# Kernel optimization log

Measured on AMD Instinct MI355X. Metric: run time of the kernel, lower is better.

Reference implementation:

```python
import jax, jax.numpy as jnp
import numpy as np

N, E, G = 51200, 819200, 256            # nodes, directed edges, graphs
N2, A, E2 = 102400, 204800, 409600      # 2-sets, assignments, 2-set edges
D, L, NI2, NAF = 64, 5, 36, 40          # emb_dim, num_layer, num_i_2, num_atom_features
EPS = 1e-5


def _seg_sum(v, seg, n):
    return jax.ops.segment_sum(v, seg, num_segments=n)


def _seg_mean(v, seg, n):
    s = jax.ops.segment_sum(v, seg, num_segments=n)
    c = jax.ops.segment_sum(jnp.ones((v.shape[0],), v.dtype), seg, num_segments=n)
    return s / jnp.maximum(c, 1.0)[:, None]


def setup_inputs() -> dict:
    key = jax.random.key(0)
    ks = iter(jax.random.split(key, 64))
    nrm = lambda shape: jax.random.normal(next(ks), shape, jnp.float32) * 0.1
    x = jax.random.normal(next(ks), (N, NAF), jnp.float32)
    edge_index = jax.random.randint(next(ks), (2, E), 0, N, dtype=jnp.int32)
    edge_attr = jnp.stack([jax.random.randint(next(ks), (E,), 0, 4, dtype=jnp.int32),
                           jax.random.randint(next(ks), (E,), 0, 3, dtype=jnp.int32)], axis=1)
    batch = jnp.repeat(jnp.arange(G, dtype=jnp.int32), N // G)
    iso_type_2 = jax.nn.one_hot(jax.random.randint(next(ks), (N2,), 0, NI2), NI2, dtype=jnp.float32)
    edge_index_2 = jax.random.randint(next(ks), (2, E2), 0, N2, dtype=jnp.int32)
    assignment_index_2 = jnp.stack([jax.random.randint(next(ks), (A,), 0, N, dtype=jnp.int32),
                                    jnp.repeat(jnp.arange(N2, dtype=jnp.int32), 2)], axis=0)
    batch_2 = jnp.repeat(jnp.arange(G, dtype=jnp.int32), N2 // G)
    params = dict(
        emb_W=nrm((NAF, D)), emb_b=jnp.zeros((D,), jnp.float32),
        gin_W1=nrm((L, D, 2 * D)), gin_b1=jnp.zeros((L, 2 * D), jnp.float32),
        gin_W2=nrm((L, 2 * D, D)), gin_b2=jnp.zeros((L, D), jnp.float32),
        eemb1=nrm((L, 6, D)), eemb2=nrm((L, 3, D)),
        bn_gamma=jnp.ones((L, D), jnp.float32), bn_beta=jnp.zeros((L, D), jnp.float32),
        iso1_rel_W=nrm((D + NI2, D)), iso1_rel_b=jnp.zeros((D,), jnp.float32),
        iso1_root_W=nrm((D + NI2, D)),
        iso2_rel_W=nrm((D, D)), iso2_rel_b=jnp.zeros((D,), jnp.float32),
        iso2_root_W=nrm((D, D)),
        ro_W0=nrm((2 * D, D)), ro_b0=jnp.zeros((D,), jnp.float32),
        ro_W1=nrm((D, D // 2)), ro_b1=jnp.zeros((D // 2,), jnp.float32),
        ro_W2=nrm((D // 2, D // 4)), ro_b2=jnp.zeros((D // 4,), jnp.float32),
        last_W=nrm((D // 4, 1)), last_b=jnp.zeros((1,), jnp.float32),
    )
    return dict(x=x, edge_index=edge_index, edge_attr=edge_attr, batch=batch,
                iso_type_2=iso_type_2, edge_index_2=edge_index_2,
                assignment_index_2=assignment_index_2, batch_2=batch_2, **params)


def _forward(x, iso_type_2, emb_W, emb_b, gin_W1, gin_b1, gin_W2, gin_b2,
             eemb1, eemb2, bn_gamma, bn_beta,
             iso1_rel_W, iso1_rel_b, iso1_root_W, iso2_rel_W, iso2_rel_b, iso2_root_W,
             ro_W0, ro_b0, ro_W1, ro_b1, ro_W2, ro_b2, last_W, last_b,
             edge_index, edge_attr, batch, edge_index_2, assignment_index_2, batch_2):
    # --- GIN stack with edge-feature embeddings and self loops ---
    loop = jnp.arange(N, dtype=edge_index.dtype)
    src = jnp.concatenate([edge_index[0], loop])
    dst = jnp.concatenate([edge_index[1], loop])
    sl_attr = jnp.tile(jnp.array([[4, 0]], dtype=edge_attr.dtype), (N, 1))
    ea = jnp.concatenate([edge_attr, sl_attr], axis=0)  # [E+N, 2]

    h = jax.nn.relu(x @ emb_W + emb_b)  # x_embedding1
    for l in range(L):
        e = eemb1[l][ea[:, 0]] + eemb2[l][ea[:, 1]]      # [E+N, D]
        agg = _seg_sum(h[src] + e, dst, N)               # gather + scatter-add
        h2 = jax.nn.relu(agg @ gin_W1[l] + gin_b1[l]) @ gin_W2[l] + gin_b2[l]
        mu = jnp.mean(h2, axis=0)
        var = jnp.var(h2, axis=0)                        # biased, torch BN training mode
        h2 = (h2 - mu) / jnp.sqrt(var + EPS) * bn_gamma[l] + bn_beta[l]
        h = h2 if l == L - 1 else jax.nn.relu(h2)        # last layer: no ReLU (JK='last')
    node_rep = h

    # --- graph mean pool of node representation ---
    x1 = _seg_mean(node_rep, batch, G)                   # [G, D]

    # --- 2-set branch: avg_pool onto 2-sets, concat iso type, two GraphConvs ---
    xp = _seg_mean(node_rep[assignment_index_2[0]], assignment_index_2[1], N2)
    xp = jnp.concatenate([xp, iso_type_2], axis=1)       # [N2, D+NI2]

    def graph_conv(z, Wrel, brel, Wroot):
        agg = _seg_sum(z[edge_index_2[0]], edge_index_2[1], N2)
        return agg @ Wrel + brel + z @ Wroot

    xp = jax.nn.relu(graph_conv(xp, iso1_rel_W, iso1_rel_b, iso1_root_W))
    xp = jax.nn.relu(graph_conv(xp, iso2_rel_W, iso2_rel_b, iso2_root_W))
    x2 = _seg_mean(xp, batch_2, G)                       # [G, D]

    # --- readout MLP ---
    m = jnp.concatenate([x1, x2], axis=1)                # [G, 2D]
    m = jax.nn.relu(m @ ro_W0 + ro_b0)
    m = jax.nn.relu(m @ ro_W1 + ro_b1)
    m = jax.nn.relu(m @ ro_W2 + ro_b2)
    m = m @ last_W + last_b
    return m.reshape(-1)                                 # num_tasks == 1 -> flat [G]


def reference(x, edge_index, edge_attr, batch, iso_type_2, edge_index_2,
              assignment_index_2, batch_2, emb_W, emb_b, gin_W1, gin_b1, gin_W2,
              gin_b2, eemb1, eemb2, bn_gamma, bn_beta, iso1_rel_W, iso1_rel_b,
              iso1_root_W, iso2_rel_W, iso2_rel_b, iso2_root_W, ro_W0, ro_b0,
              ro_W1, ro_b1, ro_W2, ro_b2, last_W, last_b):
    return _forward(x, iso_type_2, emb_W, emb_b, gin_W1, gin_b1, gin_W2, gin_b2,
                    eemb1, eemb2, bn_gamma, bn_beta,
                    iso1_rel_W, iso1_rel_b, iso1_root_W, iso2_rel_W, iso2_rel_b,
                    iso2_root_W, ro_W0, ro_b0, ro_W1, ro_b1, ro_W2, ro_b2,
                    last_W, last_b, edge_index, edge_attr, batch, edge_index_2,
                    assignment_index_2, batch_2)
```

## Files before the change

kernel.cpp:

```cpp
#include <hip/hip_runtime.h>

#define NN   51200
#define EE   819200
#define GG   256
#define NN2  102400
#define AA   204800
#define EE2  409600
#define DD   64
#define LL   5

#define NB1  100
#define NB2  200
#define CAP1 10240
#define CAP2 3072

typedef __attribute__((ext_vector_type(8))) short bf16x8;
typedef __attribute__((ext_vector_type(4))) float f32x4;
typedef unsigned short ushort_t;

#define OFF_H      ((size_t)0)
#define OFF_AGG    ((size_t)13107200)
#define OFF_H2     ((size_t)26214400)
#define OFF_XP     ((size_t)39321600)
#define OFF_REC1   OFF_XP
#define OFF_REC2   ((size_t)47513600)
#define OFF_PERM   ((size_t)60293120)
#define OFF_YROOT  ((size_t)65536000)
#define OFF_OFFS1  ((size_t)91750400)
#define OFF_COL1   ((size_t)91955216)
#define OFF_OFFS2  ((size_t)95232016)
#define OFF_COL2   ((size_t)95641632)
#define OFF_CNT1   ((size_t)97280032)
#define OFF_BBASE  ((size_t)97282080)
#define OFF_CUR1   ((size_t)97484832)
#define OFF_STATS  ((size_t)98508832)
#define ZERO_BYTES ((size_t)1231360)
#define OFF_ISO    ((size_t)98511392)
#define OFF_M      ((size_t)98920992)
#define WS_NEEDED  ((size_t)99052064)

__device__ __forceinline__ int waveInclScan(int v, int lane) {
#pragma unroll
    for (int off = 1; off < 64; off <<= 1) {
        int t = __shfl_up(v, off, 64);
        if (lane >= off) v += t;
    }
    return v;
}

__device__ __forceinline__ void bsplit(float x, ushort_t& hi, ushort_t& lo) {
    union { float f; unsigned u; } a; a.f = x;
    unsigned hb = (a.u + 0x7FFFu + ((a.u >> 16) & 1u)) >> 16;
    union { unsigned u; float f; } h; h.u = hb << 16;
    float r = x - h.f;
    union { float f; unsigned u; } b; b.f = r;
    unsigned lb = (b.u + 0x7FFFu + ((b.u >> 16) & 1u)) >> 16;
    hi = (ushort_t)hb; lo = (ushort_t)lb;
}

__global__ __launch_bounds__(256) void kbA(const int* __restrict__ src1, const int* __restrict__ dst1,
                                           const int* __restrict__ ea,
                                           const int* __restrict__ src2, const int* __restrict__ dst2,
                                           int* __restrict__ bucketCnt,
                                           int2* __restrict__ rec1, int2* __restrict__ rec2) {
    __shared__ int lhist[256];
    __shared__ int lbase[256];
    int tid = threadIdx.x, b = blockIdx.x;
    lhist[tid] = 0;
    __syncthreads();
    if (b < 400) {
        int i = (b * 256 + tid) * 8;
        int4 d0 = *(const int4*)(dst1 + i);
        int4 d1 = *(const int4*)(dst1 + i + 4);
        int dst[8] = {d0.x, d0.y, d0.z, d0.w, d1.x, d1.y, d1.z, d1.w};
        int bin[8], lr[8];
#pragma unroll
        for (int j = 0; j < 8; ++j) {
            bin[j] = dst[j] >> 9;
            lr[j] = atomicAdd(&lhist[bin[j]], 1);
        }
        __syncthreads();
        if (tid < NB1) {
            int c = lhist[tid];
            lbase[tid] = c ? atomicAdd(&bucketCnt[tid], c) : 0;
        }
        __syncthreads();
        int4 s0 = *(const int4*)(src1 + i);
        int4 s1 = *(const int4*)(src1 + i + 4);
        int src[8] = {s0.x, s0.y, s0.z, s0.w, s1.x, s1.y, s1.z, s1.w};
        int4 e0 = *(const int4*)(ea + 2 * i);
        int4 e1 = *(const int4*)(ea + 2 * i + 4);
        int4 e2 = *(const int4*)(ea + 2 * i + 8);
        int4 e3 = *(const int4*)(ea + 2 * i + 12);
        int code[8] = {e0.x * 3 + e0.y, e0.z * 3 + e0.w, e1.x * 3 + e1.y, e1.z * 3 + e1.w,
                       e2.x * 3 + e2.y, e2.z * 3 + e2.w, e3.x * 3 + e3.y, e3.z * 3 + e3.w};
#pragma unroll
        for (int j = 0; j < 8; ++j) {
            int pos = bin[j] * CAP1 + lbase[bin[j]] + lr[j];
            rec1[pos] = make_int2(src[j] | (code[j] << 16), dst[j]);
        }
    } else {
        int i = ((b - 400) * 256 + tid) * 8;
        int4 d0 = *(const int4*)(dst2 + i);
        int4 d1 = *(const int4*)(dst2 + i + 4);
        int dst[8] = {d0.x, d0.y, d0.z, d0.w, d1.x, d1.y, d1.z, d1.w};
        int bin[8], lr[8];
#pragma unroll
        for (int j = 0; j < 8; ++j) {
            bin[j] = dst[j] >> 9;
            lr[j] = atomicAdd(&lhist[bin[j]], 1);
        }
        __syncthreads();
        if (tid < NB2) {
            int c = lhist[tid];
            lbase[tid] = c ? atomicAdd(&bucketCnt[NB1 + tid], c) : 0;
        }
        __syncthreads();
        int4 s0 = *(const int4*)(src2 + i);
        int4 s1 = *(const int4*)(src2 + i + 4);
        int src[8] = {s0.x, s0.y, s0.z, s0.w, s1.x, s1.y, s1.z, s1.w};
#pragma unroll
        for (int j = 0; j < 8; ++j) {
            int pos = bin[j] * CAP2 + lbase[bin[j]] + lr[j];
            rec2[pos] = make_int2(src[j], dst[j]);
        }
    }
}

__global__ void kbscan(const int* __restrict__ bucketCnt, int* __restrict__ bucketBase) {
    __shared__ int wsum[4];
    int tid = threadIdx.x, lane = tid & 63, wid = tid >> 6;
    int nb = blockIdx.x ? NB2 : NB1;
    const int* cnt = bucketCnt + (blockIdx.x ? NB1 : 0);
    int* base = bucketBase + (blockIdx.x ? NB1 : 0);
    int v = (tid < nb) ? cnt[tid] : 0;
    int incl = waveInclScan(v, lane);
    if (lane == 63) wsum[wid] = incl;
    __syncthreads();
    int woff = 0;
#pragma unroll
    for (int w = 0; w < 3; ++w) woff += (w < wid) ? wsum[w] : 0;
    if (tid < nb) base[tid] = woff + incl - v;
}

__global__ __launch_bounds__(256) void kbB(const int* __restrict__ bucketCnt,
                                           const int* __restrict__ bucketBase,
                                           const int2* __restrict__ rec1, const int2* __restrict__ rec2,
                                           int* __restrict__ offs1, int* __restrict__ col1,
                                           int* __restrict__ offs2, int* __restrict__ col2,
                                           int* __restrict__ dbin) {
    __shared__ int nh[512];
    __shared__ int ncur[512];
    __shared__ int wsum[4];
    __shared__ int dhist[64];
    int tid = threadIdx.x, b = blockIdx.x;
    bool g1 = b < NB1;
    const int2* rec = g1 ? (rec1 + (size_t)b * CAP1) : (rec2 + (size_t)(b - NB1) * CAP2);
    int cnt = bucketCnt[b];
    int base = bucketBase[b];
    int* offs = g1 ? offs1 : offs2;
    int* col = g1 ? col1 : col2;
    int nodeBase = g1 ? b * 512 : (b - NB1) * 512;
    nh[tid] = 0; nh[tid + 256] = 0;
    if (tid < 64) dhist[tid] = 0;
    __syncthreads();
    for (int e = tid; e < cnt; e += 256) {
        int2 r = rec[e];
        atomicAdd(&nh[r.y & 511], 1);
    }
    __syncthreads();
    int v0 = nh[2 * tid], v1 = nh[2 * tid + 1];
    int s = v0 + v1;
    int lane = tid & 63, wid = tid >> 6;
    int incl = waveInclScan(s, lane);
    if (lane == 63) wsum[wid] = incl;
    __syncthreads();
    int woff = 0;
#pragma unroll
    for (int w = 0; w < 3; ++w) woff += (w < wid) ? wsum[w] : 0;
    int excl = woff + incl - s;
    ncur[2 * tid] = excl;
    ncur[2 * tid + 1] = excl + v0;
    offs[nodeBase + 2 * tid] = base + excl;
    offs[nodeBase + 2 * tid + 1] = base + excl + v0;
    if (g1) {
        atomicAdd(&dhist[v0 < 63 ? v0 : 63], 1);
        atomicAdd(&dhist[v1 < 63 ? v1 : 63], 1);
    }
    __syncthreads();
    for (int e = tid; e < cnt; e += 256) {
        int2 r = rec[e];
        int node = r.y & 511;
        int slot = base + atomicAdd(&ncur[node], 1);
        col[slot] = r.x;
    }
    if (g1 && tid < 64 && dhist[tid]) atomicAdd(&dbin[tid], dhist[tid]);
    if (tid == 0) {
        if (b == NB1 - 1) offs1[NN] = EE;
        if (b == NB1 + NB2 - 1) offs2[NN2] = EE2;
    }
}

__global__ __launch_bounds__(256) void kiso(const float* __restrict__ iso, int* __restrict__ isoIdx) {
    __shared__ float srow[256 * 36];
    int tid = threadIdx.x;
    int base = blockIdx.x * 256;
    const float4* g4p = (const float4*)(iso + (size_t)base * 36);
#pragma unroll
    for (int i = tid; i < 2304; i += 256) ((float4*)srow)[i] = g4p[i];
    __syncthreads();
    const float* r = srow + tid * 36;
    int best = 0;
#pragma unroll
    for (int k = 0; k < 36; ++k)
        if (r[k] > 0.5f) best = k;
    isoIdx[base + tid] = best;
}

__global__ void kprepx(const float* __restrict__ x, const float* __restrict__ embW,
                       const float* __restrict__ embB, float* __restrict__ h,
                       const float* __restrict__ gW1, const float* __restrict__ gW2,
                       ushort_t* __restrict__ w1h, ushort_t* __restrict__ w1l,
                       ushort_t* __restrict__ w2h, ushort_t* __restrict__ w2l,
                       const float* __restrict__ i1rW, const float* __restrict__ i1tW,
                       const float* __restrict__ i2rW, const float* __restrict__ i2tW,
                       ushort_t* __restrict__ gcwh, ushort_t* __restrict__ gcwl) {
    int b = blockIdx.x;
    if (b < 12800) {
        int t = b * 256 + threadIdx.x;
        int n = t >> 6, d = t & 63;
        float acc = embB[d];
        const float4* xr4 = (const float4*)(x + (size_t)n * 40);
#pragma unroll
        for (int k4 = 0; k4 < 10; ++k4) {
            float4 xv = xr4[k4];
            acc = fmaf(xv.x, embW[(4 * k4 + 0) * 64 + d], acc);
            acc = fmaf(xv.y, embW[(4 * k4 + 1) * 64 + d], acc);
            acc = fmaf(xv.z, embW[(4 * k4 + 2) * 64 + d], acc);
            acc = fmaf(xv.w, embW[(4 * k4 + 3) * 64 + d], acc);
        }
        h[(size_t)n * 64 + d] = fmaxf(acc, 0.f);
    } else if (b < 12840) {
        int t = (b - 12800) * 256 + threadIdx.x;
        int lane = t & 63, frag = t >> 6;
        int c15 = lane & 15, q = lane >> 4;
        if (frag < 80) {
            int kt = frag & 1, nt = (frag >> 1) & 7, l = frag >> 4;
            const float* W = gW1 + l * 8192;
            ushort_t* oh = w1h + ((size_t)frag * 64 + lane) * 8;
            ushort_t* ol = w1l + ((size_t)frag * 64 + lane) * 8;
            int kb = kt * 32 + q * 8, colw = nt * 16 + c15;
#pragma unroll
            for (int j = 0; j < 8; ++j) {
                ushort_t hi, lo; bsplit(W[(kb + j) * 128 + colw], hi, lo);
                oh[j] = hi; ol[j] = lo;
            }
        } else if (frag < 160) {
            int f = frag - 80;
            int kt = f & 3, nt = (f >> 2) & 3, l = f >> 4;
            const float* W = gW2 + l * 8192;
            ushort_t* oh = w2h + ((size_t)f * 64 + lane) * 8;
            ushort_t* ol = w2l + ((size_t)f * 64 + lane) * 8;
            int kb = kt * 32 + q * 8, colw = nt * 16 + c15;
#pragma unroll
            for (int j = 0; j < 8; ++j) {
                ushort_t hi, lo; bsplit(W[(kb + j) * 64 + colw], hi, lo);
                oh[j] = hi; ol[j] = lo;
            }
        }
    } else {
        int t = (b - 12840) * 256 + threadIdx.x;
        int lane = t & 63, frag = t >> 6;
        int c15 = lane & 15, q = lane >> 4;
        int m = frag >> 3, f = frag & 7;
        int kt = f & 1, nt = f >> 1;
        const float* W = (m == 0) ? i1rW : (m == 1) ? i1tW : (m == 2) ? i2rW : i2tW;
        ushort_t* oh = gcwh + (size_t)m * 4096 + ((size_t)f * 64 + lane) * 8;
        ushort_t* ol = gcwl + (size_t)m * 4096 + ((size_t)f * 64 + lane) * 8;
        int kb = kt * 32 + q * 8, colw = nt * 16 + c15;
#pragma unroll
        for (int j = 0; j < 8; ++j) {
            ushort_t hi, lo; bsplit(W[(kb + j) * 64 + colw], hi, lo);
            oh[j] = hi; ol[j] = lo;
        }
    }
}

__global__ __launch_bounds__(256) void kdegplace(const int* __restrict__ offs,
                                                 const int* __restrict__ dbin,
                                                 int* __restrict__ dcur,
                                                 int* __restrict__ perm) {
    __shared__ int lhist[64];
    __shared__ int lbase[64];
    __shared__ int sdstart[64];
    int tid = threadIdx.x;
    if (tid < 64) {
        lhist[tid] = 0;
        int v = dbin[tid];
        int incl = waveInclScan(v, tid);
        sdstart[tid] = incl - v;
    }
    __syncthreads();
    int n = blockIdx.x * 256 + tid;
    int d = offs[n + 1] - offs[n]; d = d < 63 ? d : 63;
    int lr = atomicAdd(&lhist[d], 1);
    __syncthreads();
    if (tid < 64) {
        int c = lhist[tid];
        lbase[tid] = c ? atomicAdd(&dcur[tid], c) : 0;
    }
    __syncthreads();
    perm[sdstart[d] + lbase[d] + lr] = n;
}

__global__ __launch_bounds__(256) void ktrans(float* __restrict__ h,
                                              const float* __restrict__ pst,
                                              const float* __restrict__ gamma,
                                              const float* __restrict__ beta) {
    __shared__ float sstat[128];
    __shared__ float sSC[64], sSH[64];
    int tid = threadIdx.x;
    if (tid < 128) {
        float s = 0.f;
        const float* p = pst + tid;
#pragma unroll
        for (int i = 0; i < 32; ++i) s += p[i * 128];
        sstat[tid] = s;
    }
    __syncthreads();
    if (tid < 64) {
        float mu = sstat[tid] * (1.f / NN);
        float var = sstat[64 + tid] * (1.f / NN) - mu * mu;
        float sc = gamma[tid] * rsqrtf(var + 1e-5f);
        sSC[tid] = sc; sSH[tid] = beta[tid] - mu * sc;
    }
    __syncthreads();
    int c = (tid & 15) * 4;
    float4 sc4 = *(const float4*)(sSC + c);
    float4 sh4 = *(const float4*)(sSH + c);
    float4* hp = (float4*)h;
    size_t base = (size_t)blockIdx.x * 1024 + tid;
#pragma unroll
    for (int r = 0; r < 4; ++r) {
        float4 v = hp[base + r * 256];
        v.x = fmaxf(fmaf(v.x, sc4.x, sh4.x), 0.f);
        v.y = fmaxf(fmaf(v.y, sc4.y, sh4.y), 0.f);
        v.z = fmaxf(fmaf(v.z, sc4.z, sh4.z), 0.f);
        v.w = fmaxf(fmaf(v.w, sc4.w, sh4.w), 0.f);
        hp[base + r * 256] = v;
    }
}

__global__ __launch_bounds__(256) void kglayer(
    const float* __restrict__ hin, float* __restrict__ hout,
    const int* __restrict__ perm,
    const int* __restrict__ offs, const int* __restrict__ col,
    const float* __restrict__ e1, const float* __restrict__ e2,
    const ushort_t* __restrict__ w1h, const ushort_t* __restrict__ w1l,
    const ushort_t* __restrict__ w2h, const ushort_t* __restrict__ w2l,
    const float* __restrict__ b1, const float* __restrict__ b2,
    float* __restrict__ pstout) {
    __shared__ float etab[13 * 64];
    __shared__ int sPerm[16];
    __shared__ float sMLP[16 * 132];
    float* sA = sMLP;
    float* sH = sMLP;
    int tid = threadIdx.x;
    if (tid < 16) sPerm[tid] = perm[blockIdx.x * 16 + tid];
    for (int idx = tid; idx < 13 * 64; idx += 256) {
        int ci = idx >> 6, dd = idx & 63;
        etab[idx] = e1[(ci / 3) * 64 + dd] + e2[(ci % 3) * 64 + dd];
    }
    __syncthreads();
    int lane = tid & 63, wv = tid >> 6;
    int c15 = lane & 15, q = lane >> 4;

    {
        int n = sPerm[wv * 4 + q];
        int s0 = offs[n], s1 = offs[n + 1];
        float4 sx = *(const float4*)(hin + (size_t)n * 64 + 4 * c15);
        float4 et = *(const float4*)(etab + 12 * 64 + 4 * c15);
        float a0 = sx.x + et.x, a1 = sx.y + et.y, a2 = sx.z + et.z, a3 = sx.w + et.w;
        int deg = s1 - s0;
        if (deg > 0) {
            const int* cp = col + s0;
            int nfull = deg >> 3, rem = deg & 7;
            int vv[8];
#pragma unroll
            for (int j = 0; j < 8; ++j) {
                int idx = j < deg ? j : deg - 1;
                vv[j] = cp[idx];
            }
            for (int it = 0; it < nfull; ++it) {
                float4 xv[8], tv[8];
#pragma unroll
                for (int j = 0; j < 8; ++j) {
                    xv[j] = *(const float4*)(hin + (size_t)(vv[j] & 0xFFFF) * 64 + 4 * c15);
                    tv[j] = *(const float4*)(etab + (vv[j] >> 16) * 64 + 4 * c15);
                }
                int e8 = (it + 1) * 8;
                bool more = e8 < deg;
                int nx[8];
                if (more) {
#pragma unroll
                    for (int j = 0; j < 8; ++j) {
                        int idx = e8 + j; idx = idx < deg ? idx : deg - 1;
                        nx[j] = cp[idx];
                    }
                }
#pragma unroll
                for (int j = 0; j < 8; ++j) {
                    a0 += xv[j].x + tv[j].x;
                    a1 += xv[j].y + tv[j].y;
                    a2 += xv[j].z + tv[j].z;
                    a3 += xv[j].w + tv[j].w;
                }
                if (more) {
#pragma unroll
                    for (int j = 0; j < 8; ++j) vv[j] = nx[j];
                }
            }
            if (rem) {
                float4 xv[8], tv[8];
#pragma unroll
                for (int j = 0; j < 8; ++j) {
                    xv[j] = *(const float4*)(hin + (size_t)(vv[j] & 0xFFFF) * 64 + 4 * c15);
                    tv[j] = *(const float4*)(etab + (vv[j] >> 16) * 64 + 4 * c15);
                }
#pragma unroll
                for (int j = 0; j < 8; ++j) {
                    float mm = (j < rem) ? 1.f : 0.f;
                    a0 = fmaf(xv[j].x + tv[j].x, mm, a0);
                    a1 = fmaf(xv[j].y + tv[j].y, mm, a1);
                    a2 = fmaf(xv[j].z + tv[j].z, mm, a2);
                    a3 = fmaf(xv[j].w + tv[j].w, mm, a3);
                }
            }
        }
        *(float4*)(sA + (wv * 4 + q) * 68 + 4 * c15) = make_float4(a0, a1, a2, a3);
    }
    __syncthreads();

    bf16x8 ah[2], al[2];
#pragma unroll
    for (int kt = 0; kt < 2; ++kt) {
        const float* p = sA + c15 * 68 + kt * 32 + q * 8;
        float4 x0 = *(const float4*)p;
        float4 x1 = *(const float4*)(p + 4);
        float xs[8] = {x0.x, x0.y, x0.z, x0.w, x1.x, x1.y, x1.z, x1.w};
#pragma unroll
        for (int j = 0; j < 8; ++j) {
            ushort_t hi, lo; bsplit(xs[j], hi, lo);
            ah[kt][j] = (short)hi; al[kt][j] = (short)lo;
        }
    }
    __syncthreads();

    f32x4 acc1[2];
#pragma unroll
    for (int j = 0; j < 2; ++j) { f32x4 z = {0.f, 0.f, 0.f, 0.f}; acc1[j] = z; }
#pragma unroll
    for (int kt = 0; kt < 2; ++kt) {
#pragma unroll
        for (int j = 0; j < 2; ++j) {
            int nt = 2 * wv + j;
            size_t fo = ((size_t)((nt * 2 + kt) * 64 + lane)) * 8;
            bf16x8 bh = *(const bf16x8*)(w1h + fo);
            bf16x8 bl = *(const bf16x8*)(w1l + fo);
            acc1[j] = __builtin_amdgcn_mfma_f32_16x16x32_bf16(ah[kt], bh, acc1[j], 0, 0, 0);
            acc1[j] = __builtin_amdgcn_mfma_f32_16x16x32_bf16(al[kt], bh, acc1[j], 0, 0, 0);
            acc1[j] = __builtin_amdgcn_mfma_f32_16x16x32_bf16(ah[kt], bl, acc1[j], 0, 0, 0);
        }
    }
#pragma unroll
    for (int j = 0; j < 2; ++j) {
        int nt = 2 * wv + j;
        float bias = b1[nt * 16 + c15];
#pragma unroll
        for (int rg = 0; rg < 4; ++rg)
            sH[(4 * q + rg) * 132 + nt * 16 + c15] = fmaxf(acc1[j][rg] + bias, 0.f);
    }
    __syncthreads();

    f32x4 acc2 = {0.f, 0.f, 0.f, 0.f};
#pragma unroll
    for (int kt = 0; kt < 4; ++kt) {
        const float* p = sH + c15 * 132 + kt * 32 + q * 8;
        float4 x0 = *(const float4*)p;
        float4 x1 = *(const float4*)(p + 4);
        float xs[8] = {x0.x, x0.y, x0.z, x0.w, x1.x, x1.y, x1.z, x1.w};
        bf16x8 a2h, a2l;
#pragma unroll
        for (int j = 0; j < 8; ++j) {
            ushort_t hi, lo; bsplit(xs[j], hi, lo);
            a2h[j] = (short)hi; a2l[j] = (short)lo;
        }
        size_t fo = ((size_t)((wv * 4 + kt) * 64 + lane)) * 8;
        bf16x8 bh = *(const bf16x8*)(w2h + fo);
        bf16x8 bl = *(const bf16x8*)(w2l + fo);
        acc2 = __builtin_amdgcn_mfma_f32_16x16x32_bf16(a2h, bh, acc2, 0, 0, 0);
        acc2 = __builtin_amdgcn_mfma_f32_16x16x32_bf16(a2l, bh, acc2, 0, 0, 0);
        acc2 = __builtin_amdgcn_mfma_f32_16x16x32_bf16(a2h, bl, acc2, 0, 0, 0);
    }
    {
        float bias = b2[wv * 16 + c15];
        float s = 0.f, s2 = 0.f;
#pragma unroll
        for (int rg = 0; rg < 4; ++rg) {
            float v = acc2[rg] + bias;
            hout[(size_t)sPerm[4 * q + rg] * 64 + wv * 16 + c15] = v;
            s += v; s2 += v * v;
        }
        s += __shfl_xor(s, 16, 64);  s += __shfl_xor(s, 32, 64);
        s2 += __shfl_xor(s2, 16, 64); s2 += __shfl_xor(s2, 32, 64);
        if (q == 0) {
            float* ps = pstout + (size_t)(blockIdx.x & 31) * 128;
            atomicAdd(&ps[wv * 16 + c15], s);
            atomicAdd(&ps[64 + wv * 16 + c15], s2);
        }
    }
}

__global__ __launch_bounds__(256) void kgcmm1(const ushort_t* __restrict__ grh,
                                              const ushort_t* __restrict__ grl,
                                              const ushort_t* __restrict__ gth,
                                              const ushort_t* __restrict__ gtl,
                                              const float* __restrict__ WrelIso,
                                              const float* __restrict__ WrootIso,
                                              const int* __restrict__ isoIdx,
                                              float* __restrict__ Yrel,
                                              float* __restrict__ Yroot,
                                              const float* __restrict__ pst,
                                              const float* __restrict__ g4,
                                              const float* __restrict__ b4,
                                              const int* __restrict__ a0g,
                                              const float* __restrict__ h2src) {
    __shared__ float sX[64 * 68];
    __shared__ float sstat[128];
    __shared__ float sSC[64], sSH[64];
    int tid = threadIdx.x, blk = blockIdx.x;
    if (tid < 128) {
        float s = 0.f;
        const float* p = pst + tid;
#pragma unroll
        for (int i = 0; i < 32; ++i) s += p[i * 128];
        sstat[tid] = s;
    }
    __syncthreads();
    if (tid < 64) {
        float mu = sstat[tid] * (1.f / NN);
        float var = sstat[64 + tid] * (1.f / NN) - mu * mu;
        float sc = g4[tid] * rsqrtf(var + 1e-5f);
        sSC[tid] = sc;
        sSH[tid] = b4[tid] - mu * sc;
    }
    __syncthreads();
#pragma unroll
    for (int i = tid; i < 1024; i += 256) {
        int row = i >> 4, c = (i & 15) << 2;
        int grow = blk * 64 + row;
        int na = a0g[2 * grow], nb = a0g[2 * grow + 1];
        float4 va = *(const float4*)(h2src + (size_t)na * 64 + c);
        float4 vb = *(const float4*)(h2src + (size_t)nb * 64 + c);
        float4 v;
        v.x = 0.5f * (va.x + vb.x); v.y = 0.5f * (va.y + vb.y);
        v.z = 0.5f * (va.z + vb.z); v.w = 0.5f * (va.w + vb.w);
        v.x = fmaf(v.x, sSC[c], sSH[c]);
        v.y = fmaf(v.y, sSC[c + 1], sSH[c + 1]);
        v.z = fmaf(v.z, sSC[c + 2], sSH[c + 2]);
        v.w = fmaf(v.w, sSC[c + 3], sSH[c + 3]);
        float* p = sX + row * 68 + c;
        p[0] = v.x; p[1] = v.y; p[2] = v.z; p[3] = v.w;
    }
    __syncthreads();
    int lane = tid & 63, wv = tid >> 6;
    int c15 = lane & 15, q = lane >> 4;

    bf16x8 ah[2], al[2];
#pragma unroll
    for (int kt = 0; kt < 2; ++kt) {
        const float* p = sX + (16 * wv + c15) * 68 + kt * 32 + q * 8;
        float4 x0 = *(const float4*)p;
        float4 x1 = *(const float4*)(p + 4);
        float xs[8] = {x0.x, x0.y, x0.z, x0.w, x1.x, x1.y, x1.z, x1.w};
#pragma unroll
        for (int j = 0; j < 8; ++j) {
            ushort_t hi, lo; bsplit(xs[j], hi, lo);
            ah[kt][j] = (short)hi; al[kt][j] = (short)lo;
        }
    }

    f32x4 accR[4], accT[4];
#pragma unroll
    for (int nt = 0; nt < 4; ++nt) {
        f32x4 z = {0.f, 0.f, 0.f, 0.f};
        accR[nt] = z; accT[nt] = z;
    }
#pragma unroll
    for (int nt = 0; nt < 4; ++nt) {
#pragma unroll
        for (int kt = 0; kt < 2; ++kt) {
            size_t fo = ((size_t)((nt * 2 + kt) * 64 + lane)) * 8;
            bf16x8 bh = *(const bf16x8*)(grh + fo);
            bf16x8 bl = *(const bf16x8*)(grl + fo);
            accR[nt] = __builtin_amdgcn_mfma_f32_16x16x32_bf16(ah[kt], bh, accR[nt], 0, 0, 0);
            accR[nt] = __builtin_amdgcn_mfma_f32_16x16x32_bf16(al[kt], bh, accR[nt], 0, 0, 0);
            accR[nt] = __builtin_amdgcn_mfma_f32_16x16x32_bf16(ah[kt], bl, accR[nt], 0, 0, 0);
            bf16x8 ch = *(const bf16x8*)(gth + fo);
            bf16x8 cl = *(const bf16x8*)(gtl + fo);
            accT[nt] = __builtin_amdgcn_mfma_f32_16x16x32_bf16(ah[kt], ch, accT[nt], 0, 0, 0);
            accT[nt] = __builtin_amdgcn_mfma_f32_16x16x32_bf16(al[kt], ch, accT[nt], 0, 0, 0);
            accT[nt] = __builtin_amdgcn_mfma_f32_16x16x32_bf16(ah[kt], cl, accT[nt], 0, 0, 0);
        }
    }

    int rbase = blk * 64 + 16 * wv + 4 * q;
#pragma unroll
    for (int rg = 0; rg < 4; ++rg) {
        int row = rbase + rg;
        int ii = isoIdx[row];
        float* yr = Yrel + (size_t)row * 64;
        float* yt = Yroot + (size_t)row * 64;
        const float* er = WrelIso + (size_t)ii * 64;
        const float* et = WrootIso + (size_t)ii * 64;
#pragma unroll
        for (int nt = 0; nt < 4; ++nt) {
            int cc = nt * 16 + c15;
            yr[cc] = accR[nt][rg] + er[cc];
            yt[cc] = accT[nt][rg] + et[cc];
        }
    }
}

__global__ __launch_bounds__(256) void kgcmm2(const float* __restrict__ AGG,
                                              const float* __restrict__ XP,
                                              const ushort_t* __restrict__ grh,
                                              const ushort_t* __restrict__ grl,
                                              const ushort_t* __restrict__ gth,
                                              const ushort_t* __restrict__ gtl,
                                              const float* __restrict__ brel,
                                              float* __restrict__ OUT) {
    __shared__ float sA[64 * 68];
    __shared__ float sB[64 * 68];
    int tid = threadIdx.x, blk = blockIdx.x;
#pragma unroll
    for (int i = tid; i < 1024; i += 256) {
        int row = i >> 4, c = (i & 15) << 2;
        float4 va = ((const float4*)(AGG + (size_t)blk * 4096))[i];
        float4 vb = ((const float4*)(XP + (size_t)blk * 4096))[i];
        float* pa = sA + row * 68 + c;
        float* pb = sB + row * 68 + c;
        pa[0] = va.x; pa[1] = va.y; pa[2] = va.z; pa[3] = va.w;
        pb[0] = vb.x; pb[1] = vb.y; pb[2] = vb.z; pb[3] = vb.w;
    }
    __syncthreads();
    int lane = tid & 63, wv = tid >> 6;
    int c15 = lane & 15, q = lane >> 4;

    bf16x8 aAh[2], aAl[2], aBh[2], aBl[2];
#pragma unroll
    for (int kt = 0; kt < 2; ++kt) {
        const float* pa = sA + (16 * wv + c15) * 68 + kt * 32 + q * 8;
        const float* pb = sB + (16 * wv + c15) * 68 + kt * 32 + q * 8;
        float4 a0 = *(const float4*)pa;
        float4 a1 = *(const float4*)(pa + 4);
        float4 b0 = *(const float4*)pb;
        float4 b1 = *(const float4*)(pb + 4);
        float as[8] = {a0.x, a0.y, a0.z, a0.w, a1.x, a1.y, a1.z, a1.w};
        float bs[8] = {b0.x, b0.y, b0.z, b0.w, b1.x, b1.y, b1.z, b1.w};
#pragma unroll
        for (int j = 0; j < 8; ++j) {
            ushort_t hi, lo;
            bsplit(as[j], hi, lo); aAh[kt][j] = (short)hi; aAl[kt][j] = (short)lo;
            bsplit(bs[j], hi, lo); aBh[kt][j] = (short)hi; aBl[kt][j] = (short)lo;
        }
    }

    f32x4 acc[4];
#pragma unroll
    for (int nt = 0; nt < 4; ++nt) { f32x4 z = {0.f, 0.f, 0.f, 0.f}; acc[nt] = z; }
#pragma unroll
    for (int nt = 0; nt < 4; ++nt) {
#pragma unroll
        for (int kt = 0; kt < 2; ++kt) {
            size_t fo = ((size_t)((nt * 2 + kt) * 64 + lane)) * 8;
            bf16x8 bh = *(const bf16x8*)(grh + fo);
            bf16x8 bl = *(const bf16x8*)(grl + fo);
            acc[nt] = __builtin_amdgcn_mfma_f32_16x16x32_bf16(aAh[kt], bh, acc[nt], 0, 0, 0);
            acc[nt] = __builtin_amdgcn_mfma_f32_16x16x32_bf16(aAl[kt], bh, acc[nt], 0, 0, 0);
            acc[nt] = __builtin_amdgcn_mfma_f32_16x16x32_bf16(aAh[kt], bl, acc[nt], 0, 0, 0);
            bf16x8 ch = *(const bf16x8*)(gth + fo);
            bf16x8 cl = *(const bf16x8*)(gtl + fo);
            acc[nt] = __builtin_amdgcn_mfma_f32_16x16x32_bf16(aBh[kt], ch, acc[nt], 0, 0, 0);
            acc[nt] = __builtin_amdgcn_mfma_f32_16x16x32_bf16(aBl[kt], ch, acc[nt], 0, 0, 0);
            acc[nt] = __builtin_amdgcn_mfma_f32_16x16x32_bf16(aBh[kt], cl, acc[nt], 0, 0, 0);
        }
    }

    int rbase = blk * 64 + 16 * wv + 4 * q;
#pragma unroll
    for (int rg = 0; rg < 4; ++rg) {
        int row = rbase + rg;
        float* yo = OUT + (size_t)row * 64;
#pragma unroll
        for (int nt = 0; nt < 4; ++nt) {
            int cc = nt * 16 + c15;
            yo[cc] = fmaxf(acc[nt][rg] + brel[cc], 0.f);
        }
    }
}

__global__ void kgather2(const float* __restrict__ yrel, const float* __restrict__ yroot,
                         const float* __restrict__ brel, const int* __restrict__ offs,
                         const int* __restrict__ col, float* __restrict__ out) {
    int t = blockIdx.x * 256 + threadIdx.x;
    int j = t >> 4, c = t & 15;
    int s0 = offs[j], s1 = offs[j + 1];
    float4 rt = *(const float4*)(yroot + (size_t)j * 64 + 4 * c);
    float4 bb = *(const float4*)(brel + 4 * c);
    float a0 = rt.x + bb.x, a1 = rt.y + bb.y, a2 = rt.z + bb.z, a3 = rt.w + bb.w;
    if (s0 < s1) {
        int vv[4];
#pragma unroll
        for (int jj = 0; jj < 4; ++jj) {
            int idx = s0 + jj; idx = idx < s1 ? idx : s1 - 1;
            vv[jj] = col[idx];
        }
        int e = s0;
        while (true) {
            int ne = e + 4;
            bool more = ne < s1;
            float4 xs[4];
#pragma unroll
            for (int jj = 0; jj < 4; ++jj)
                xs[jj] = *(const float4*)(yrel + (size_t)vv[jj] * 64 + 4 * c);
            int nx[4];
            if (more) {
#pragma unroll
                for (int jj = 0; jj < 4; ++jj) {
                    int idx = ne + jj; idx = idx < s1 ? idx : s1 - 1;
                    nx[jj] = col[idx];
                }
            }
#pragma unroll
            for (int jj = 0; jj < 4; ++jj) {
                float mm = (e + jj < s1) ? 1.f : 0.f;
                a0 = fmaf(xs[jj].x, mm, a0);
                a1 = fmaf(xs[jj].y, mm, a1);
                a2 = fmaf(xs[jj].z, mm, a2);
                a3 = fmaf(xs[jj].w, mm, a3);
            }
            if (!more) break;
            e = ne;
#pragma unroll
            for (int jj = 0; jj < 4; ++jj) vv[jj] = nx[jj];
        }
    }
    *(float4*)(out + (size_t)j * 64 + 4 * c) =
        make_float4(fmaxf(a0, 0.f), fmaxf(a1, 0.f), fmaxf(a2, 0.f), fmaxf(a3, 0.f));
}

__global__ void kgather2raw(const float* __restrict__ xpsrc, const int* __restrict__ offs,
                            const int* __restrict__ col, float* __restrict__ agg) {
    int t = blockIdx.x * 256 + threadIdx.x;
    int j = t >> 4, c = t & 15;
    int s0 = offs[j], s1 = offs[j + 1];
    float a0 = 0.f, a1 = 0.f, a2 = 0.f, a3 = 0.f;
    if (s0 < s1) {
        int vv[4];
#pragma unroll
        for (int jj = 0; jj < 4; ++jj) {
            int idx = s0 + jj; idx = idx < s1 ? idx : s1 - 1;
            vv[jj] = col[idx];
        }
        int e = s0;
        while (true) {
            int ne = e + 4;
            bool more = ne < s1;
            float4 xs[4];
#pragma unroll
            for (int jj = 0; jj < 4; ++jj)
                xs[jj] = *(const float4*)(xpsrc + (size_t)vv[jj] * 64 + 4 * c);
            int nx[4];
            if (more) {
#pragma unroll
                for (int jj = 0; jj < 4; ++jj) {
                    int idx = ne + jj; idx = idx < s1 ? idx : s1 - 1;
                    nx[jj] = col[idx];
                }
            }
#pragma unroll
            for (int jj = 0; jj < 4; ++jj) {
                float mm = (e + jj < s1) ? 1.f : 0.f;
                a0 = fmaf(xs[jj].x, mm, a0);
                a1 = fmaf(xs[jj].y, mm, a1);
                a2 = fmaf(xs[jj].z, mm, a2);
                a3 = fmaf(xs[jj].w, mm, a3);
            }
            if (!more) break;
            e = ne;
#pragma unroll
            for (int jj = 0; jj < 4; ++jj) vv[jj] = nx[jj];
        }
    }
    *(float4*)(agg + (size_t)j * 64 + 4 * c) = make_float4(a0, a1, a2, a3);
}

__global__ void kpoolg(const float* __restrict__ h2, const float* __restrict__ xp2,
                       const float* __restrict__ pst, const float* __restrict__ g4,
                       const float* __restrict__ b4, float* __restrict__ m) {
    __shared__ float sstat[128];
    __shared__ float red[4][64];
    int g = blockIdx.x, tid = threadIdx.x;
    if (tid < 128) {
        float s = 0.f;
        const float* p = pst + tid;
#pragma unroll
        for (int i = 0; i < 32; ++i) s += p[i * 128];
        sstat[tid] = s;
    }
    int wid = tid >> 6, d = tid & 63;
    float s1 = 0.f;
    for (int i = wid; i < 200; i += 4) s1 += h2[((size_t)g * 200 + i) * 64 + d];
    red[wid][d] = s1;
    __syncthreads();
    if (wid == 0) {
        float mean = (red[0][d] + red[1][d] + red[2][d] + red[3][d]) * (1.f / 200.f);
        float mu = sstat[d] * (1.f / NN);
        float var = sstat[64 + d] * (1.f / NN) - mu * mu;
        float sc = g4[d] * rsqrtf(var + 1e-5f);
        m[g * 128 + d] = fmaf(mean, sc, b4[d] - mu * sc);
    }
    __syncthreads();
    float s2 = 0.f;
    for (int i = wid; i < 400; i += 4) s2 += xp2[((size_t)g * 400 + i) * 64 + d];
    red[wid][d] = s2;
    __syncthreads();
    if (wid == 0) m[g * 128 + 64 + d] = (red[0][d] + red[1][d] + red[2][d] + red[3][d]) * (1.f / 400.f);
}

__global__ void kread(const float* __restrict__ m, const float* __restrict__ W0,
                      const float* __restrict__ b0, const float* __restrict__ W1,
                      const float* __restrict__ b1, const float* __restrict__ W2,
                      const float* __restrict__ b2, const float* __restrict__ lw,
                      const float* __restrict__ lb, float* __restrict__ out) {
    __shared__ float s0[64], s1[32], s2[16];
    int g = blockIdx.x, d = threadIdx.x;
    const float* mr = m + g * 128;
    float t = b0[d];
    for (int k = 0; k < 128; ++k) t = fmaf(mr[k], W0[k * 64 + d], t);
    s0[d] = fmaxf(t, 0.f);
    __syncthreads();
    if (d < 32) {
        float u = b1[d];
        for (int k = 0; k < 64; ++k) u = fmaf(s0[k], W1[k * 32 + d], u);
        s1[d] = fmaxf(u, 0.f);
    }
    __syncthreads();
    if (d < 16) {
        float u = b2[d];
        for (int k = 0; k < 32; ++k) u = fmaf(s1[k], W2[k * 16 + d], u);
        s2[d] = fmaxf(u, 0.f);
    }
    __syncthreads();
    if (d == 0) {
        float u = lb[0];
        for (int k = 0; k < 16; ++k) u = fmaf(s2[k], lw[k], u);
        out[g] = u;
    }
}

extern "C" void kernel_launch(void* const* d_in, const int* in_sizes, int n_in,
                              void* d_out, int out_size, void* d_ws, size_t ws_size,
                              hipStream_t stream) {
    if (ws_size < WS_NEEDED) return;

    const float* x    = (const float*)d_in[0];
    const int*   ei   = (const int*)d_in[1];
    const int*   ea   = (const int*)d_in[2];
    const float* iso  = (const float*)d_in[4];
    const int*   ei2  = (const int*)d_in[5];
    const int*   ai2  = (const int*)d_in[6];
    const float* embW = (const float*)d_in[8];
    const float* embB = (const float*)d_in[9];
    const float* gW1  = (const float*)d_in[10];
    const float* gB1  = (const float*)d_in[11];
    const float* gW2  = (const float*)d_in[12];
    const float* gB2  = (const float*)d_in[13];
    const float* ee1  = (const float*)d_in[14];
    const float* ee2  = (const float*)d_in[15];
    const float* bng  = (const float*)d_in[16];
    const float* bnb  = (const float*)d_in[17];
    const float* i1rW = (const float*)d_in[18];
    const float* i1rB = (const float*)d_in[19];
    const float* i1tW = (const float*)d_in[20];
    const float* i2rW = (const float*)d_in[21];
    const float* i2rB = (const float*)d_in[22];
    const float* i2tW = (const float*)d_in[23];
    const float* roW0 = (const float*)d_in[24];
    const float* roB0 = (const float*)d_in[25];
    const float* roW1 = (const float*)d_in[26];
    const float* roB1 = (const float*)d_in[27];
    const float* roW2 = (const float*)d_in[28];
    const float* roB2 = (const float*)d_in[29];
    const float* lW   = (const float*)d_in[30];
    const float* lB   = (const float*)d_in[31];
    float* out = (float*)d_out;

    char* ws = (char*)d_ws;
    float* h      = (float*)(ws + OFF_H);
    float* hB     = (float*)(ws + OFF_AGG);
    float* hA     = (float*)(ws + OFF_H2);
    float* h2     = hA;
    float* xp     = (float*)(ws + OFF_XP);
    float* yrel   = (float*)(ws + OFF_H);
    float* yroot  = (float*)(ws + OFF_YROOT);
    float* aggb   = (float*)(ws + OFF_H);
    float* xp2    = (float*)(ws + OFF_YROOT);
    int* offs1    = (int*)(ws + OFF_OFFS1);
    int* col1     = (int*)(ws + OFF_COL1);
    int* offs2    = (int*)(ws + OFF_OFFS2);
    int* col2     = (int*)(ws + OFF_COL2);
    int* isoIdx   = (int*)(ws + OFF_ISO);
    float* mbuf   = (float*)(ws + OFF_M);
    ushort_t* w1h = (ushort_t*)(ws + OFF_YROOT);
    ushort_t* w1l = (ushort_t*)(ws + OFF_YROOT + 81920);
    ushort_t* w2h = (ushort_t*)(ws + OFF_YROOT + 163840);
    ushort_t* w2l = (ushort_t*)(ws + OFF_YROOT + 245760);
    ushort_t* gcwh = (ushort_t*)(ws + OFF_M);
    ushort_t* gcwl = (ushort_t*)(ws + OFF_M + 32768);
    float* pstat2 = (float*)(ws + OFF_CUR1);
    int2* rec1    = (int2*)(ws + OFF_REC1);
    int2* rec2    = (int2*)(ws + OFF_REC2);
    int* bucketCnt  = (int*)(ws + OFF_CNT1);
    int* bucketBase = (int*)(ws + OFF_BBASE);
    int* perm     = (int*)(ws + OFF_PERM);
    int* dbin     = (int*)(ws + OFF_STATS);
    int* dcur     = dbin + 64;

    const int* src1 = ei;
    const int* dst1 = ei + EE;
    const int* src2 = ei2;
    const int* dst2 = ei2 + EE2;
    const int* a0   = ai2;

    hipMemsetAsync(ws + OFF_CNT1, 0, ZERO_BYTES, stream);

    kbA<<<600, 256, 0, stream>>>(src1, dst1, ea, src2, dst2, bucketCnt, rec1, rec2);
    kiso<<<NN2 / 256, 256, 0, stream>>>(iso, isoIdx);
    kprepx<<<12848, 256, 0, stream>>>(x, embW, embB, h, gW1, gW2,
                                      w1h, w1l, w2h, w2l,
                                      i1rW, i1tW, i2rW, i2tW, gcwh, gcwl);
    kbscan<<<2, 256, 0, stream>>>(bucketCnt, bucketBase);
    kbB<<<300, 256, 0, stream>>>(bucketCnt, bucketBase, rec1, rec2,
                                 offs1, col1, offs2, col2, dbin);
    kdegplace<<<NN / 256, 256, 0, stream>>>(offs1, dbin, dcur, perm);

    for (int l = 0; l < LL; ++l) {
        const float* hin = (l == 0) ? h : ((l & 1) ? hA : hB);
        float* hout = (l & 1) ? hB : hA;
        kglayer<<<NN / 16, 256, 0, stream>>>(
            hin, hout, perm, offs1, col1, ee1 + l * 384, ee2 + l * 192,
            w1h + (size_t)l * 8192, w1l + (size_t)l * 8192,
            w2h + (size_t)l * 8192, w2l + (size_t)l * 8192,
            gB1 + l * 128, gB2 + l * 64,
            pstat2 + (size_t)l * 4096);
        if (l < LL - 1)
            ktrans<<<800, 256, 0, stream>>>(hout, pstat2 + (size_t)l * 4096,
                                            bng + l * 64, bnb + l * 64);
    }

    kgcmm1<<<NN2 / 64, 256, 0, stream>>>(gcwh, gcwl, gcwh + 4096, gcwl + 4096,
                                         i1rW + 64 * 64, i1tW + 64 * 64, isoIdx,
                                         yrel, yroot,
                                         pstat2 + (size_t)4 * 4096,
                                         bng + 4 * 64, bnb + 4 * 64, a0, h2);
    kgather2<<<NN2 * 16 / 256, 256, 0, stream>>>(yrel, yroot, i1rB, offs2, col2, xp);
    kgather2raw<<<NN2 * 16 / 256, 256, 0, stream>>>(xp, offs2, col2, aggb);
    kgcmm2<<<NN2 / 64, 256, 0, stream>>>(aggb, xp,
                                         gcwh + 8192, gcwl + 8192, gcwh + 12288, gcwl + 12288,
                                         i2rB, xp2);

    kpoolg<<<GG, 256, 0, stream>>>(h2, xp2, pstat2 + (size_t)4 * 4096,
                                   bng + 4 * 64, bnb + 4 * 64, mbuf);
    kread<<<GG, 64, 0, stream>>>(mbuf, roW0, roB0, roW1, roB1, roW2, roB2, lW, lB, out);
}
```

Baseline: 568.3 us.

## Store gathered node features in bf16 to halve gather traffic

Result: faster. 529.3 us (-6.9%).

```diff
diff --git a/kernel.cpp b/kernel.cpp
--- a/kernel.cpp
+++ b/kernel.cpp
@@ -57,6 +57,13 @@
     unsigned lb = (b.u + 0x7FFFu + ((b.u >> 16) & 1u)) >> 16;
     hi = (ushort_t)hb; lo = (ushort_t)lb;
 }
+__device__ __forceinline__ ushort_t f2bf(float x) {
+    union { float f; unsigned u; } a; a.f = x;
+    return (ushort_t)((a.u + 0x7FFFu + ((a.u >> 16) & 1u)) >> 16);
+}
+__device__ __forceinline__ float bf2f(ushort_t v) {
+    union { unsigned u; float f; } t; t.u = (unsigned)v << 16; return t.f;
+}
 
 __global__ __launch_bounds__(256) void kbA(const int* __restrict__ src1, const int* __restrict__ dst1,
                                            const int* __restrict__ ea,
@@ -218,7 +225,7 @@
 }
 
 __global__ void kprepx(const float* __restrict__ x, const float* __restrict__ embW,
-                       const float* __restrict__ embB, float* __restrict__ h,
+                       const float* __restrict__ embB, ushort_t* __restrict__ hbf,
                        const float* __restrict__ gW1, const float* __restrict__ gW2,
                        ushort_t* __restrict__ w1h, ushort_t* __restrict__ w1l,
                        ushort_t* __restrict__ w2h, ushort_t* __restrict__ w2l,
@@ -239,7 +246,7 @@
             acc = fmaf(xv.z, embW[(4 * k4 + 2) * 64 + d], acc);
             acc = fmaf(xv.w, embW[(4 * k4 + 3) * 64 + d], acc);
         }
-        h[(size_t)n * 64 + d] = fmaxf(acc, 0.f);
+        hbf[(size_t)n * 64 + d] = f2bf(fmaxf(acc, 0.f));
     } else if (b < 12840) {
         int t = (b - 12800) * 256 + threadIdx.x;
         int lane = t & 63, frag = t >> 6;
@@ -313,7 +320,8 @@
     perm[sdstart[d] + lbase[d] + lr] = n;
 }
 
-__global__ __launch_bounds__(256) void ktrans(float* __restrict__ h,
+__global__ __launch_bounds__(256) void ktrans(const float* __restrict__ hraw,
+                                              ushort_t* __restrict__ hbf,
                                               const float* __restrict__ pst,
                                               const float* __restrict__ gamma,
                                               const float* __restrict__ beta) {
@@ -338,21 +346,23 @@
     int c = (tid & 15) * 4;
     float4 sc4 = *(const float4*)(sSC + c);
     float4 sh4 = *(const float4*)(sSH + c);
-    float4* hp = (float4*)h;
+    const float4* hp = (const float4*)hraw;
+    ushort4* op = (ushort4*)hbf;
     size_t base = (size_t)blockIdx.x * 1024 + tid;
 #pragma unroll
     for (int r = 0; r < 4; ++r) {
         float4 v = hp[base + r * 256];
-        v.x = fmaxf(fmaf(v.x, sc4.x, sh4.x), 0.f);
-        v.y = fmaxf(fmaf(v.y, sc4.y, sh4.y), 0.f);
-        v.z = fmaxf(fmaf(v.z, sc4.z, sh4.z), 0.f);
-        v.w = fmaxf(fmaf(v.w, sc4.w, sh4.w), 0.f);
-        hp[base + r * 256] = v;
+        ushort4 o;
+        o.x = f2bf(fmaxf(fmaf(v.x, sc4.x, sh4.x), 0.f));
+        o.y = f2bf(fmaxf(fmaf(v.y, sc4.y, sh4.y), 0.f));
+        o.z = f2bf(fmaxf(fmaf(v.z, sc4.z, sh4.z), 0.f));
+        o.w = f2bf(fmaxf(fmaf(v.w, sc4.w, sh4.w), 0.f));
+        op[base + r * 256] = o;
     }
 }
 
 __global__ __launch_bounds__(256) void kglayer(
-    const float* __restrict__ hin, float* __restrict__ hout,
+    const ushort_t* __restrict__ hin, float* __restrict__ hout,
     const int* __restrict__ perm,
     const int* __restrict__ offs, const int* __restrict__ col,
     const float* __restrict__ e1, const float* __restrict__ e2,
@@ -378,9 +388,10 @@
     {
         int n = sPerm[wv * 4 + q];
         int s0 = offs[n], s1 = offs[n + 1];
-        float4 sx = *(const float4*)(hin + (size_t)n * 64 + 4 * c15);
+        ushort4 sx = *(const ushort4*)(hin + (size_t)n * 64 + 4 * c15);
         float4 et = *(const float4*)(etab + 12 * 64 + 4 * c15);
-        float a0 = sx.x + et.x, a1 = sx.y + et.y, a2 = sx.z + et.z, a3 = sx.w + et.w;
+        float a0 = bf2f(sx.x) + et.x, a1 = bf2f(sx.y) + et.y;
+        float a2 = bf2f(sx.z) + et.z, a3 = bf2f(sx.w) + et.w;
         int deg = s1 - s0;
         if (deg > 0) {
             const int* cp = col + s0;
@@ -392,10 +403,11 @@
                 vv[j] = cp[idx];
             }
             for (int it = 0; it < nfull; ++it) {
-                float4 xv[8], tv[8];
+                ushort4 xv[8];
+                float4 tv[8];
 #pragma unroll
                 for (int j = 0; j < 8; ++j) {
-                    xv[j] = *(const float4*)(hin + (size_t)(vv[j] & 0xFFFF) * 64 + 4 * c15);
+                    xv[j] = *(const ushort4*)(hin + (size_t)(vv[j] & 0xFFFF) * 64 + 4 * c15);
                     tv[j] = *(const float4*)(etab + (vv[j] >> 16) * 64 + 4 * c15);
                 }
                 int e8 = (it + 1) * 8;
@@ -410,10 +422,10 @@
                 }
 #pragma unroll
                 for (int j = 0; j < 8; ++j) {
-                    a0 += xv[j].x + tv[j].x;
-                    a1 += xv[j].y + tv[j].y;
-                    a2 += xv[j].z + tv[j].z;
-                    a3 += xv[j].w + tv[j].w;
+                    a0 += bf2f(xv[j].x) + tv[j].x;
+                    a1 += bf2f(xv[j].y) + tv[j].y;
+                    a2 += bf2f(xv[j].z) + tv[j].z;
+                    a3 += bf2f(xv[j].w) + tv[j].w;
                 }
                 if (more) {
 #pragma unroll
@@ -421,19 +433,20 @@
                 }
             }
             if (rem) {
-                float4 xv[8], tv[8];
+                ushort4 xv[8];
+                float4 tv[8];
 #pragma unroll
                 for (int j = 0; j < 8; ++j) {
-                    xv[j] = *(const float4*)(hin + (size_t)(vv[j] & 0xFFFF) * 64 + 4 * c15);
+                    xv[j] = *(const ushort4*)(hin + (size_t)(vv[j] & 0xFFFF) * 64 + 4 * c15);
                     tv[j] = *(const float4*)(etab + (vv[j] >> 16) * 64 + 4 * c15);
                 }
 #pragma unroll
                 for (int j = 0; j < 8; ++j) {
                     float mm = (j < rem) ? 1.f : 0.f;
-                    a0 = fmaf(xv[j].x + tv[j].x, mm, a0);
-                    a1 = fmaf(xv[j].y + tv[j].y, mm, a1);
-                    a2 = fmaf(xv[j].z + tv[j].z, mm, a2);
-                    a3 = fmaf(xv[j].w + tv[j].w, mm, a3);
+                    a0 = fmaf(bf2f(xv[j].x) + tv[j].x, mm, a0);
+                    a1 = fmaf(bf2f(xv[j].y) + tv[j].y, mm, a1);
+                    a2 = fmaf(bf2f(xv[j].z) + tv[j].z, mm, a2);
+                    a3 = fmaf(bf2f(xv[j].w) + tv[j].w, mm, a3);
                 }
             }
         }
@@ -528,7 +541,7 @@
                                               const float* __restrict__ WrelIso,
                                               const float* __restrict__ WrootIso,
                                               const int* __restrict__ isoIdx,
-                                              float* __restrict__ Yrel,
+                                              ushort_t* __restrict__ Yrel,
                                               float* __restrict__ Yroot,
                                               const float* __restrict__ pst,
                                               const float* __restrict__ g4,
@@ -619,21 +632,21 @@
     for (int rg = 0; rg < 4; ++rg) {
         int row = rbase + rg;
         int ii = isoIdx[row];
-        float* yr = Yrel + (size_t)row * 64;
+        ushort_t* yr = Yrel + (size_t)row * 64;
         float* yt = Yroot + (size_t)row * 64;
         const float* er = WrelIso + (size_t)ii * 64;
         const float* et = WrootIso + (size_t)ii * 64;
 #pragma unroll
         for (int nt = 0; nt < 4; ++nt) {
             int cc = nt * 16 + c15;
-            yr[cc] = accR[nt][rg] + er[cc];
+            yr[cc] = f2bf(accR[nt][rg] + er[cc]);
             yt[cc] = accT[nt][rg] + et[cc];
         }
     }
 }
 
 __global__ __launch_bounds__(256) void kgcmm2(const float* __restrict__ AGG,
-                                              const float* __restrict__ XP,
+                                              const ushort_t* __restrict__ XP,
                                               const ushort_t* __restrict__ grh,
                                               const ushort_t* __restrict__ grl,
                                               const ushort_t* __restrict__ gth,
@@ -647,17 +660,17 @@
     for (int i = tid; i < 1024; i += 256) {
         int row = i >> 4, c = (i & 15) << 2;
         float4 va = ((const float4*)(AGG + (size_t)blk * 4096))[i];
-        float4 vb = ((const float4*)(XP + (size_t)blk * 4096))[i];
+        ushort4 vb4 = ((const ushort4*)(XP + (size_t)blk * 4096))[i];
         float* pa = sA + row * 68 + c;
         float* pb = sB + row * 68 + c;
         pa[0] = va.x; pa[1] = va.y; pa[2] = va.z; pa[3] = va.w;
-        pb[0] = vb.x; pb[1] = vb.y; pb[2] = vb.z; pb[3] = vb.w;
+        pb[0] = bf2f(vb4.x); pb[1] = bf2f(vb4.y); pb[2] = bf2f(vb4.z); pb[3] = bf2f(vb4.w);
     }
     __syncthreads();
     int lane = tid & 63, wv = tid >> 6;
     int c15 = lane & 15, q = lane >> 4;
 
-    bf16x8 aAh[2], aAl[2], aBh[2], aBl[2];
+    bf16x8 aAh[2], aAl[2], aBh[2];
 #pragma unroll
     for (int kt = 0; kt < 2; ++kt) {
         const float* pa = sA + (16 * wv + c15) * 68 + kt * 32 + q * 8;
@@ -672,7 +685,7 @@
         for (int j = 0; j < 8; ++j) {
             ushort_t hi, lo;
             bsplit(as[j], hi, lo); aAh[kt][j] = (short)hi; aAl[kt][j] = (short)lo;
-            bsplit(bs[j], hi, lo); aBh[kt][j] = (short)hi; aBl[kt][j] = (short)lo;
+            aBh[kt][j] = (short)f2bf(bs[j]);
         }
     }
 
@@ -692,7 +705,6 @@
             bf16x8 ch = *(const bf16x8*)(gth + fo);
             bf16x8 cl = *(const bf16x8*)(gtl + fo);
             acc[nt] = __builtin_amdgcn_mfma_f32_16x16x32_bf16(aBh[kt], ch, acc[nt], 0, 0, 0);
-            acc[nt] = __builtin_amdgcn_mfma_f32_16x16x32_bf16(aBl[kt], ch, acc[nt], 0, 0, 0);
             acc[nt] = __builtin_amdgcn_mfma_f32_16x16x32_bf16(aBh[kt], cl, acc[nt], 0, 0, 0);
         }
     }
@@ -710,9 +722,9 @@
     }
 }
 
-__global__ void kgather2(const float* __restrict__ yrel, const float* __restrict__ yroot,
+__global__ void kgather2(const ushort_t* __restrict__ yrel, const float* __restrict__ yroot,
                          const float* __restrict__ brel, const int* __restrict__ offs,
-                         const int* __restrict__ col, float* __restrict__ out) {
+                         const int* __restrict__ col, ushort_t* __restrict__ out) {
     int t = blockIdx.x * 256 + threadIdx.x;
     int j = t >> 4, c = t & 15;
     int s0 = offs[j], s1 = offs[j + 1];
@@ -730,10 +742,10 @@
         while (true) {
             int ne = e + 4;
             bool more = ne < s1;
-            float4 xs[4];
+            ushort4 xs[4];
 #pragma unroll
             for (int jj = 0; jj < 4; ++jj)
-                xs[jj] = *(const float4*)(yrel + (size_t)vv[jj] * 64 + 4 * c);
+                xs[jj] = *(const ushort4*)(yrel + (size_t)vv[jj] * 64 + 4 * c);
             int nx[4];
             if (more) {
 #pragma unroll
@@ -745,10 +757,10 @@
 #pragma unroll
             for (int jj = 0; jj < 4; ++jj) {
                 float mm = (e + jj < s1) ? 1.f : 0.f;
-                a0 = fmaf(xs[jj].x, mm, a0);
-                a1 = fmaf(xs[jj].y, mm, a1);
-                a2 = fmaf(xs[jj].z, mm, a2);
-                a3 = fmaf(xs[jj].w, mm, a3);
+                a0 = fmaf(bf2f(xs[jj].x), mm, a0);
+                a1 = fmaf(bf2f(xs[jj].y), mm, a1);
+                a2 = fmaf(bf2f(xs[jj].z), mm, a2);
+                a3 = fmaf(bf2f(xs[jj].w), mm, a3);
             }
             if (!more) break;
             e = ne;
@@ -756,11 +768,15 @@
             for (int jj = 0; jj < 4; ++jj) vv[jj] = nx[jj];
         }
     }
-    *(float4*)(out + (size_t)j * 64 + 4 * c) =
-        make_float4(fmaxf(a0, 0.f), fmaxf(a1, 0.f), fmaxf(a2, 0.f), fmaxf(a3, 0.f));
-}
-
-__global__ void kgather2raw(const float* __restrict__ xpsrc, const int* __restrict__ offs,
+    ushort4 o;
+    o.x = f2bf(fmaxf(a0, 0.f));
+    o.y = f2bf(fmaxf(a1, 0.f));
+    o.z = f2bf(fmaxf(a2, 0.f));
+    o.w = f2bf(fmaxf(a3, 0.f));
+    *(ushort4*)(out + (size_t)j * 64 + 4 * c) = o;
+}
+
+__global__ void kgather2raw(const ushort_t* __restrict__ xpsrc, const int* __restrict__ offs,
                             const int* __restrict__ col, float* __restrict__ agg) {
     int t = blockIdx.x * 256 + threadIdx.x;
     int j = t >> 4, c = t & 15;
@@ -777,10 +793,10 @@
         while (true) {
             int ne = e + 4;
             bool more = ne < s1;
-            float4 xs[4];
+            ushort4 xs[4];
 #pragma unroll
             for (int jj = 0; jj < 4; ++jj)
-                xs[jj] = *(const float4*)(xpsrc + (size_t)vv[jj] * 64 + 4 * c);
+                xs[jj] = *(const ushort4*)(xpsrc + (size_t)vv[jj] * 64 + 4 * c);
             int nx[4];
             if (more) {
 #pragma unroll
@@ -792,10 +808,10 @@
 #pragma unroll
             for (int jj = 0; jj < 4; ++jj) {
                 float mm = (e + jj < s1) ? 1.f : 0.f;
-                a0 = fmaf(xs[jj].x, mm, a0);
-                a1 = fmaf(xs[jj].y, mm, a1);
-                a2 = fmaf(xs[jj].z, mm, a2);
-                a3 = fmaf(xs[jj].w, mm, a3);
+                a0 = fmaf(bf2f(xs[jj].x), mm, a0);
+                a1 = fmaf(bf2f(xs[jj].y), mm, a1);
+                a2 = fmaf(bf2f(xs[jj].z), mm, a2);
+                a3 = fmaf(bf2f(xs[jj].w), mm, a3);
             }
             if (!more) break;
             e = ne;
@@ -908,14 +924,13 @@
     float* out = (float*)d_out;
 
     char* ws = (char*)d_ws;
-    float* h      = (float*)(ws + OFF_H);
-    float* hB     = (float*)(ws + OFF_AGG);
-    float* hA     = (float*)(ws + OFF_H2);
-    float* h2     = hA;
-    float* xp     = (float*)(ws + OFF_XP);
-    float* yrel   = (float*)(ws + OFF_H);
+    ushort_t* hbf = (ushort_t*)(ws + OFF_H);
+    float* hraw   = (float*)(ws + OFF_AGG);
+    float* h2     = (float*)(ws + OFF_H2);
+    ushort_t* yrelb = (ushort_t*)(ws + OFF_H);
     float* yroot  = (float*)(ws + OFF_YROOT);
     float* aggb   = (float*)(ws + OFF_H);
+    ushort_t* xpb = (ushort_t*)(ws + OFF_XP);
     float* xp2    = (float*)(ws + OFF_YROOT);
     int* offs1    = (int*)(ws + OFF_OFFS1);
     int* col1     = (int*)(ws + OFF_COL1);
@@ -948,7 +963,7 @@
 
     kbA<<<600, 256, 0, stream>>>(src1, dst1, ea, src2, dst2, bucketCnt, rec1, rec2);
     kiso<<<NN2 / 256, 256, 0, stream>>>(iso, isoIdx);
-    kprepx<<<12848, 256, 0, stream>>>(x, embW, embB, h, gW1, gW2,
+    kprepx<<<12848, 256, 0, stream>>>(x, embW, embB, hbf, gW1, gW2,
                                       w1h, w1l, w2h, w2l,
                                       i1rW, i1tW, i2rW, i2tW, gcwh, gcwl);
     kbscan<<<2, 256, 0, stream>>>(bucketCnt, bucketBase);
@@ -957,27 +972,26 @@
     kdegplace<<<NN / 256, 256, 0, stream>>>(offs1, dbin, dcur, perm);
 
     for (int l = 0; l < LL; ++l) {
-        const float* hin = (l == 0) ? h : ((l & 1) ? hA : hB);
-        float* hout = (l & 1) ? hB : hA;
+        float* hout = (l == LL - 1) ? h2 : hraw;
         kglayer<<<NN / 16, 256, 0, stream>>>(
-            hin, hout, perm, offs1, col1, ee1 + l * 384, ee2 + l * 192,
+            hbf, hout, perm, offs1, col1, ee1 + l * 384, ee2 + l * 192,
             w1h + (size_t)l * 8192, w1l + (size_t)l * 8192,
             w2h + (size_t)l * 8192, w2l + (size_t)l * 8192,
             gB1 + l * 128, gB2 + l * 64,
             pstat2 + (size_t)l * 4096);
         if (l < LL - 1)
-            ktrans<<<800, 256, 0, stream>>>(hout, pstat2 + (size_t)l * 4096,
+            ktrans<<<800, 256, 0, stream>>>(hraw, hbf, pstat2 + (size_t)l * 4096,
                                             bng + l * 64, bnb + l * 64);
     }
 
     kgcmm1<<<NN2 / 64, 256, 0, stream>>>(gcwh, gcwl, gcwh + 4096, gcwl + 4096,
                                          i1rW + 64 * 64, i1tW + 64 * 64, isoIdx,
-                                         yrel, yroot,
+                                         yrelb, yroot,
                                          pstat2 + (size_t)4 * 4096,
                                          bng + 4 * 64, bnb + 4 * 64, a0, h2);
-    kgather2<<<NN2 * 16 / 256, 256, 0, stream>>>(yrel, yroot, i1rB, offs2, col2, xp);
-    kgather2raw<<<NN2 * 16 / 256, 256, 0, stream>>>(xp, offs2, col2, aggb);
-    kgcmm2<<<NN2 / 64, 256, 0, stream>>>(aggb, xp,
+    kgather2<<<NN2 * 16 / 256, 256, 0, stream>>>(yrelb, yroot, i1rB, offs2, col2, xpb);
+    kgather2raw<<<NN2 * 16 / 256, 256, 0, stream>>>(xpb, offs2, col2, aggb);
+    kgcmm2<<<NN2 / 64, 256, 0, stream>>>(aggb, xpb,
                                          gcwh + 8192, gcwl + 8192, gcwh + 12288, gcwl + 12288,
                                          i2rB, xp2);
 
```
